# Kernel tuning notes

Measured on AMD Instinct MI355X. Metric: run time of the kernel, lower is better.

Reference implementation:

```python
import jax, jax.numpy as jnp
import numpy as np

H, N_PATCH, F, DIM = 12, 196, 8, 768
DH = DIM // H            # 64
D3 = 3 * DH              # per-head dim after 3*dim projection = 192
SCALE = float(np.sqrt(DH) * H)
B, S = 8, 1 + N_PATCH * F  # 1569


def setup_inputs() -> dict:
    key = jax.random.key(0)
    ks = jax.random.split(key, 12)
    w = lambda k, shp: (jax.random.normal(k, shp, dtype=jnp.float32) * 0.02)
    return {
        "x": jax.random.normal(ks[0], (B, S, DIM), dtype=jnp.float32),
        "Wq": w(ks[1], (DIM, 3 * DIM)), "bq": jnp.zeros((3 * DIM,), jnp.float32),
        "Wk": w(ks[2], (DIM, 3 * DIM)), "bk": jnp.zeros((3 * DIM,), jnp.float32),
        "Wv": w(ks[3], (DIM, 3 * DIM)), "bv": jnp.zeros((3 * DIM,), jnp.float32),
        "Wt": w(ks[4], (3 * DIM, DIM)), "bt": jnp.zeros((DIM,), jnp.float32),
        "Wf": w(ks[5], (3 * DIM, DIM)), "bf": jnp.zeros((DIM,), jnp.float32),
    }


def _heads(t):
    # [b, s, 3*dim] -> [b, H, s, D3]
    b, s, _ = t.shape
    return t.reshape(b, s, H, D3).transpose(0, 2, 1, 3)


def _merge(t):
    # [b, H, s, D3] -> [b, s, 3*dim]
    b, _, s, _ = t.shape
    return t.transpose(0, 2, 1, 3).reshape(b, s, H * D3)


def _attn(q, k, v):
    a = jax.nn.softmax(jnp.einsum('bhqd,bhkd->bhqk', q, k) / SCALE, axis=-1)
    return jnp.einsum('bhqk,bhkd->bhqd', a, v)


def reference(x, Wq, bq, Wk, bk, Wv, bv, Wt, bt, Wf, bf):
    patches = x[:, 1:, :]                       # [b, n*F, dim]
    # NOTE: faithful to original code: v_mat comes from self.k, k_mat from self.v
    qm = _heads(patches @ Wq + bq)
    vm = _heads(patches @ Wk + bk)
    km = _heads(patches @ Wv + bv)

    # CLS attention over full sequence (here v from self.v, k from self.k)
    q_cls = _heads(x[:, 0:1, :] @ Wq + bq)      # [b,H,1,D3]
    v_cls = _heads(x @ Wv + bv)
    k_cls = _heads(x @ Wk + bk)
    inter_cls = _attn(q_cls, k_cls, v_cls)      # [b,H,1,D3]

    # Stage 1: temporal attention per patch (patches 1..n-1), vectorized.
    # tokens are frame-major: index = frame*n + patch, so slice p::n == patch p across frames
    def per_patch(t):
        b = t.shape[0]
        return t.reshape(b, H, F, N_PATCH, D3)[:, :, :, 1:, :].transpose(0, 1, 3, 2, 4)  # [b,H,n-1,F,D3]
    q5, k5, v5 = per_patch(qm), per_patch(km), per_patch(vm)
    a1 = jax.nn.softmax(jnp.einsum('bhpfd,bhpgd->bhpfg', q5, k5) / SCALE, axis=-1)
    t1 = jnp.einsum('bhpfg,bhpgd->bhpfd', a1, v5).sum(axis=3)   # [b,H,n-1,D3]
    t1 = jnp.tile(t1, (1, 1, F, 1))                              # [b,H,(n-1)*F,D3]
    ti = _merge(t1) @ Wt + bt                                    # [b,(n-1)*F,dim]

    # Stage 2 (same qkv swap as stage 1)
    q2 = _heads(ti @ Wq + bq)
    v2 = _heads(ti @ Wk + bk)
    k2 = _heads(ti @ Wv + bv)
    outs = [_attn(q2[:, :, 0:N_PATCH], k2[:, :, 0:N_PATCH], v2[:, :, 0:N_PATCH]).sum(axis=2, keepdims=True)]
    for xi in range(1, F):  # small fixed loop over num_frames
        o = _attn(q2[:, :, xi:xi + N_PATCH], k2[:, :, xi::N_PATCH], v2[:, :, xi::N_PATCH])
        outs.append(o.sum(axis=2, keepdims=True))
    t2 = jnp.concatenate(outs, axis=2)                           # [b,H,F,D3]
    t2 = jnp.tile(t2, (1, 1, N_PATCH, 1))                        # [b,H,F*n,D3]

    full = jnp.concatenate([inter_cls, t2], axis=2)              # [b,H,1+n*F,D3]
    return _merge(full) @ Wf + bf                                # [b,S,dim]
```

## Files before the change

### kernel.cpp

```cpp
#include <hip/hip_runtime.h>
#include <math.h>

#define B_    8
#define SEQ   1569
#define DIMX  768
#define H_    12
#define D3    192
#define F_    8
#define NP    196
#define P1    195
#define NCOL  2304
#define NS    6912
#define RSCALE (1.0f/96.0f)
#define NCHUNK 16
#define CH     99
#define CLS_STRIDE 196
#define PG4   49

typedef __bf16 bf16_t;
typedef bf16_t bf16x8 __attribute__((ext_vector_type(8)));
typedef float  f32x4  __attribute__((ext_vector_type(4)));

__device__ __forceinline__ void load_lds16(const bf16_t* g, bf16_t* l) {
  __builtin_amdgcn_global_load_lds(
      (const __attribute__((address_space(1))) void*)g,
      (__attribute__((address_space(3))) void*)l, 16, 0, 0);
}

__device__ __forceinline__ float block_max256(float v, float* red) {
  #pragma unroll
  for (int o = 32; o > 0; o >>= 1) v = fmaxf(v, __shfl_xor(v, o, 64));
  __syncthreads();
  if ((threadIdx.x & 63) == 0) red[threadIdx.x >> 6] = v;
  __syncthreads();
  return fmaxf(fmaxf(red[0], red[1]), fmaxf(red[2], red[3]));
}

__device__ __forceinline__ float block_sum256(float v, float* red) {
  #pragma unroll
  for (int o = 32; o > 0; o >>= 1) v += __shfl_xor(v, o, 64);
  __syncthreads();
  if ((threadIdx.x & 63) == 0) red[threadIdx.x >> 6] = v;
  __syncthreads();
  return red[0] + red[1] + red[2] + red[3];
}

__global__ __launch_bounds__(256) void concat_bias_kernel(
    const float* __restrict__ bq, const float* __restrict__ bk,
    const float* __restrict__ bv, float* __restrict__ qkvb) {
  const int i = blockIdx.x * 256 + threadIdx.x;
  if (i >= NS) return;
  float v;
  if (i < NCOL) v = bq[i];
  else if (i < 2 * NCOL) v = bk[i - NCOL];
  else v = bv[i - 2 * NCOL];
  qkvb[i] = v;
}

__global__ __launch_bounds__(256) void cast_swizzle(
    const float* __restrict__ x, bf16_t* __restrict__ out, int Mreal) {
  const int ms = blockIdx.x;
  const int wave = threadIdx.x >> 6, lane = threadIdx.x & 63;
  const int KP = DIMX / 32;
  int row = ms * 16 + (lane & 15);
  if (row >= Mreal) row = Mreal - 1;
  const int cb = (lane >> 4) * 8;
  const float* src = x + (size_t)row * DIMX + cb;
  bf16_t* dst = out + ((size_t)ms * KP) * 512 + lane * 8;
  for (int kp = wave; kp < KP; kp += 4) {
    const float4 a = *(const float4*)(src + kp * 32);
    const float4 b = *(const float4*)(src + kp * 32 + 4);
    bf16_t o8[8] = {(bf16_t)a.x, (bf16_t)a.y, (bf16_t)a.z, (bf16_t)a.w,
                    (bf16_t)b.x, (bf16_t)b.y, (bf16_t)b.z, (bf16_t)b.w};
    *(uint4*)(dst + (size_t)kp * 512) = *(uint4*)o8;
  }
}

__global__ __launch_bounds__(256) void transpose_all(
    const float* __restrict__ Wq, const float* __restrict__ Wk,
    const float* __restrict__ Wv, const float* __restrict__ Wt,
    const float* __restrict__ Wf, bf16_t* __restrict__ WqkvT,
    bf16_t* __restrict__ WtT, bf16_t* __restrict__ WfT) {
  __shared__ float t[32][33];
  const int bid = blockIdx.x;
  const int mat = bid / 1728, tt = bid % 1728;
  const float* W; bf16_t* WT; int Kd, Nd, nt, kt;
  if (mat < 3) {
    Kd = DIMX; Nd = NCOL;
    W = (mat == 0) ? Wq : ((mat == 1) ? Wk : Wv);
    WT = WqkvT + (size_t)mat * NCOL * DIMX;
    nt = tt % 72; kt = tt / 72;
  } else {
    Kd = NCOL; Nd = DIMX;
    W = (mat == 3) ? Wt : Wf;
    WT = (mat == 3) ? WtT : WfT;
    nt = tt % 24; kt = tt / 24;
  }
  const int bn = nt * 32, bk = kt * 32;
  const int KP = Kd >> 5;
  const int tx = threadIdx.x & 31, ty = threadIdx.x >> 5;
  #pragma unroll
  for (int i = 0; i < 32; i += 8)
    t[ty + i][tx] = W[(size_t)(bk + ty + i) * Nd + bn + tx];
  __syncthreads();
  const int k = bk + tx;
  #pragma unroll
  for (int i = 0; i < 32; i += 8) {
    const int n = bn + ty + i;
    const size_t off = ((size_t)(n >> 4) * KP + (k >> 5)) * 512 +
                       ((n & 15) + 16 * ((k >> 3) & 3)) * 8 + (k & 7);
    WT[off] = (bf16_t)t[tx][ty + i];
  }
}

__global__ __launch_bounds__(256) void gemm_mfma_bt(
    const bf16_t* __restrict__ A, const bf16_t* __restrict__ BT,
    const float* __restrict__ bias, void* __restrict__ C,
    int M, int N, int K, int MT, int NT, int GROUPM, int aSwz, int outBf16) {
  __shared__ bf16_t As[128 * 64];
  __shared__ bf16_t Bs[128 * 64];
  const int tid  = threadIdx.x;
  const int wave = tid >> 6, lane = tid & 63;

  const int pid   = blockIdx.x;
  const int npg   = GROUPM * NT;
  const int group = pid / npg;
  const int first_m = group * GROUPM;
  int gsm = MT - first_m; if (gsm > GROUPM) gsm = GROUPM;
  const int lpid  = pid % npg;
  const int m_tile = first_m + lpid % gsm;
  const int n_tile = lpid / gsm;
  const int row0 = m_tile * 128, col0 = n_tile * 128;

  const int KP = K >> 5;
  const bf16_t* Bpan = BT + ((size_t)(n_tile * 8 + wave * 2) * KP) * 512 + lane * 8;
  const bf16_t* Apan = A + ((size_t)(m_tile * 8 + wave * 2) * KP) * 512 + lane * 8;
  const int fr = lane & 15, kg = lane >> 4;
  int ra0 = row0 + wave * 32 + fr;
  int ra1 = ra0 + 16;
  if (ra0 >= M) ra0 = M - 1;
  if (ra1 >= M) ra1 = M - 1;
  const bf16_t* Ap0 = A + (size_t)ra0 * K + kg * 8;
  const bf16_t* Ap1 = A + (size_t)ra1 * K + kg * 8;

  const int la0 = (wave * 2 + 0) * 1024, la1 = (wave * 2 + 1) * 1024;
  const int mb = (wave & 1) * 4,  nb = (wave >> 1) * 4;
  const int m0 = (wave & 1) * 64, n0 = (wave >> 1) * 64;
  f32x4 acc[4][4] = {};

  for (int kk = 0; kk < K; kk += 64) {
    const int kp = kk >> 5;
    if (aSwz) {
      load_lds16(Apan + (size_t)kp * 512,            &As[la0]);
      load_lds16(Apan + (size_t)(kp + 1) * 512,      &As[la0 + 512]);
      load_lds16(Apan + (size_t)(KP + kp) * 512,     &As[la1]);
      load_lds16(Apan + (size_t)(KP + kp + 1) * 512, &As[la1 + 512]);
    } else {
      load_lds16(Ap0 + kk,      &As[la0]);
      load_lds16(Ap0 + kk + 32, &As[la0 + 512]);
      load_lds16(Ap1 + kk,      &As[la1]);
      load_lds16(Ap1 + kk + 32, &As[la1 + 512]);
    }
    load_lds16(Bpan + (size_t)kp * 512,            &Bs[la0]);
    load_lds16(Bpan + (size_t)(kp + 1) * 512,      &Bs[la0 + 512]);
    load_lds16(Bpan + (size_t)(KP + kp) * 512,     &Bs[la1]);
    load_lds16(Bpan + (size_t)(KP + kp + 1) * 512, &Bs[la1 + 512]);
    __syncthreads();

    #pragma unroll
    for (int h = 0; h < 2; ++h) {
      bf16x8 af[4], bfr[4];
      #pragma unroll
      for (int i = 0; i < 4; ++i) {
        af[i]  = *(const bf16x8*)&As[(mb + i) * 1024 + h * 512 + lane * 8];
        bfr[i] = *(const bf16x8*)&Bs[(nb + i) * 1024 + h * 512 + lane * 8];
      }
      #pragma unroll
      for (int i = 0; i < 4; ++i)
        #pragma unroll
        for (int j = 0; j < 4; ++j)
          acc[i][j] = __builtin_amdgcn_mfma_f32_16x16x32_bf16(
              af[i], bfr[j], acc[i][j], 0, 0, 0);
    }
    __syncthreads();
  }

  const int cc = lane & 15, cr4 = (lane >> 4) * 4;
  #pragma unroll
  for (int i = 0; i < 4; ++i) {
    #pragma unroll
    for (int j = 0; j < 4; ++j) {
      const int col = col0 + n0 + j * 16 + cc;
      const float bcol = bias[col];
      #pragma unroll
      for (int reg = 0; reg < 4; ++reg) {
        const int r = row0 + m0 + i * 16 + cr4 + reg;
        if (r < M) {
          const float v = acc[i][j][reg] + bcol;
          if (outBf16) ((bf16_t*)C)[(size_t)r * N + col] = (bf16_t)v;
          else         ((float*)C)[(size_t)r * N + col] = v;
        }
      }
    }
  }
}

__global__ __launch_bounds__(256) void xi0_scores_mfma(
    const bf16_t* __restrict__ QKV2, float* __restrict__ Smat) {
  __shared__ bf16_t As[128 * 32];
  __shared__ bf16_t Bs[128 * 32];
  const int tid  = threadIdx.x;
  const int wave = tid >> 6, lane = tid & 63;
  const int row0 = blockIdx.x * 128, col0 = blockIdx.y * 128;
  const int bh = blockIdx.z;
  const int b = bh / H_, h = bh % H_;
  const bf16_t* Abase = QKV2 + (size_t)b * P1 * NS + h * D3;
  const bf16_t* Bbase = QKV2 + (size_t)b * P1 * NS + 2 * NCOL + h * D3;

  const int fr = lane & 15, kg = lane >> 4;
  int ra0 = row0 + wave * 32 + fr;
  int ra1 = ra0 + 16;
  if (ra0 >= P1) ra0 = P1 - 1;
  if (ra1 >= P1) ra1 = P1 - 1;
  int cb0 = col0 + wave * 32 + fr;
  int cb1 = cb0 + 16;
  if (cb0 >= P1) cb0 = P1 - 1;
  if (cb1 >= P1) cb1 = P1 - 1;
  const bf16_t* Ap0 = Abase + (size_t)ra0 * NS + kg * 8;
  const bf16_t* Ap1 = Abase + (size_t)ra1 * NS + kg * 8;
  const bf16_t* Bp0 = Bbase + (size_t)cb0 * NS + kg * 8;
  const bf16_t* Bp1 = Bbase + (size_t)cb1 * NS + kg * 8;
  bf16_t* lA0 = &As[(wave * 2 + 0) * 512];
  bf16_t* lA1 = &As[(wave * 2 + 1) * 512];
  bf16_t* lB0 = &Bs[(wave * 2 + 0) * 512];
  bf16_t* lB1 = &Bs[(wave * 2 + 1) * 512];

  const int m0 = (wave & 1) * 64, n0 = (wave >> 1) * 64;
  const int mb = (wave & 1) * 4,  nb = (wave >> 1) * 4;
  f32x4 acc[4][4] = {};

  for (int k0 = 0; k0 < D3; k0 += 32) {
    load_lds16(Ap0 + k0, lA0);
    load_lds16(Ap1 + k0, lA1);
    load_lds16(Bp0 + k0, lB0);
    load_lds16(Bp1 + k0, lB1);
    __syncthreads();
    bf16x8 af[4], bfr[4];
    #pragma unroll
    for (int i = 0; i < 4; ++i) {
      af[i]  = *(const bf16x8*)&As[(mb + i) * 512 + lane * 8];
      bfr[i] = *(const bf16x8*)&Bs[(nb + i) * 512 + lane * 8];
    }
    #pragma unroll
    for (int i = 0; i < 4; ++i)
      #pragma unroll
      for (int j = 0; j < 4; ++j)
        acc[i][j] = __builtin_amdgcn_mfma_f32_16x16x32_bf16(
            af[i], bfr[j], acc[i][j], 0, 0, 0);
    __syncthreads();
  }

  float* S = Smat + (size_t)bh * P1 * P1;
  const int cc = lane & 15, cr4 = (lane >> 4) * 4;
  #pragma unroll
  for (int i = 0; i < 4; ++i)
    #pragma unroll
    for (int j = 0; j < 4; ++j) {
      const int col = col0 + n0 + j * 16 + cc;
      #pragma unroll
      for (int reg = 0; reg < 4; ++reg) {
        const int r = row0 + m0 + i * 16 + cr4 + reg;
        if (r < P1 && col < P1) S[(size_t)r * P1 + col] = acc[i][j][reg] * RSCALE;
      }
    }
}

__global__ __launch_bounds__(256) void xi0_finish_kernel(
    const float* __restrict__ Smat, const bf16_t* __restrict__ QKV2,
    bf16_t* __restrict__ FULL9b) {
  const int bh = blockIdx.x;
  const int b = bh / H_, h = bh % H_;
  __shared__ float mrow[P1], inv_l[P1], g[P1];
  const float* S = Smat + (size_t)bh * P1 * P1;
  const int tid = threadIdx.x;
  const int wave = tid >> 6, lane = tid & 63;

  for (int r = wave; r < P1; r += 4) {
    const float* Sr = S + (size_t)r * P1;
    const float s0 = Sr[lane];
    const float s1 = Sr[64 + lane];
    const float s2 = Sr[128 + lane];
    const float s3 = (lane < 3) ? Sr[192 + lane] : -1e30f;
    float m = fmaxf(fmaxf(s0, s1), fmaxf(s2, s3));
    #pragma unroll
    for (int o = 1; o < 64; o <<= 1) m = fmaxf(m, __shfl_xor(m, o, 64));
    float e = expf(s0 - m) * ((lane == 0) ? 2.f : 1.f) + expf(s1 - m) +
              expf(s2 - m) + ((lane < 3) ? expf(s3 - m) : 0.f);
    #pragma unroll
    for (int o = 1; o < 64; o <<= 1) e += __shfl_xor(e, o, 64);
    if (lane == 0) {
      mrow[r] = m;
      inv_l[r] = ((r == 0) ? 2.f : 1.f) / e;
    }
  }
  __syncthreads();
  if (tid < P1) {
    float s = 0.f;
    for (int r = 0; r < P1; ++r)
      s += expf(S[(size_t)r * P1 + tid] - mrow[r]) * inv_l[r];
    g[tid] = s * ((tid == 0) ? 2.f : 1.f);
  }
  __syncthreads();
  if (tid < D3) {
    float acc = 0.f;
    const bf16_t* vbase = QKV2 + (size_t)b * P1 * NS + NCOL + h * D3 + tid;
    for (int k = 0; k < P1; ++k)
      acc = fmaf(g[k], (float)vbase[(size_t)k * NS], acc);
    FULL9b[((size_t)b * 9 + 1) * NCOL + h * D3 + tid] = (bf16_t)acc;
  }
}

__global__ __launch_bounds__(256) void cls_part_kernel(
    const bf16_t* __restrict__ XQKV, float* __restrict__ CLSP, int b0) {
  const int h  = blockIdx.x % H_;
  const int bl = blockIdx.x / H_;
  const int b  = b0 + bl;
  const int c  = blockIdx.y;
  const int t0 = c * CH;
  const int tend = (t0 + CH < SEQ) ? t0 + CH : SEQ;
  __shared__ float qs[D3];
  __shared__ float sc[CH];
  __shared__ float red[4];
  const int tid = threadIdx.x;

  const bf16_t* Qr = XQKV + (size_t)bl * SEQ * NS + h * D3;
  if (tid < 24) {
    const bf16x8 q8 = *(const bf16x8*)(Qr + tid * 8);
    #pragma unroll
    for (int m2 = 0; m2 < 8; ++m2) qs[tid * 8 + m2] = (float)q8[m2];
  }
  __syncthreads();

  float lmax = -1e30f;
  for (int t = t0 + tid; t < tend; t += 256) {
    const bf16_t* kr = XQKV + ((size_t)bl * SEQ + t) * NS + NCOL + h * D3;
    float acc = 0.f;
    #pragma unroll 3
    for (int d = 0; d < D3; d += 8) {
      const bf16x8 k8 = *(const bf16x8*)(kr + d);
      #pragma unroll
      for (int m2 = 0; m2 < 8; ++m2) acc = fmaf(qs[d + m2], (float)k8[m2], acc);
    }
    acc *= RSCALE;
    sc[t - t0] = acc;
    lmax = fmaxf(lmax, acc);
  }
  const float m = block_max256(lmax, red);
  float lsum = 0.f;
  for (int t = t0 + tid; t < tend; t += 256) {
    const float e = expf(sc[t - t0] - m);
    sc[t - t0] = e;
    lsum += e;
  }
  const float L = block_sum256(lsum, red);
  __syncthreads();

  float* P = CLSP + ((size_t)(b * H_ + h) * NCHUNK + c) * CLS_STRIDE;
  if (tid < D3) {
    float acc = 0.f;
    const bf16_t* vbase = XQKV + ((size_t)bl * SEQ + t0) * NS + 2 * NCOL + h * D3 + tid;
    for (int t = t0; t < tend; ++t)
      acc = fmaf(sc[t - t0], (float)vbase[(size_t)(t - t0) * NS], acc);
    P[tid] = acc;
  }
  if (tid == 192) P[192] = m;
  if (tid == 193) P[193] = L;
}

__global__ __launch_bounds__(256) void cls_combine_kernel(
    const float* __restrict__ CLSP, bf16_t* __restrict__ FULL9b) {
  const int bh = blockIdx.x;
  const int tid = threadIdx.x;
  const float* P = CLSP + (size_t)bh * NCHUNK * CLS_STRIDE;

  float M = -1e30f;
  #pragma unroll
  for (int c = 0; c < NCHUNK; ++c) M = fmaxf(M, P[c * CLS_STRIDE + 192]);
  float L = 0.f;
  float w[NCHUNK];
  #pragma unroll
  for (int c = 0; c < NCHUNK; ++c) {
    w[c] = expf(P[c * CLS_STRIDE + 192] - M);
    L += P[c * CLS_STRIDE + 193] * w[c];
  }
  if (tid < D3) {
    float acc = 0.f;
    #pragma unroll
    for (int c = 0; c < NCHUNK; ++c)
      acc = fmaf(w[c], P[c * CLS_STRIDE + tid], acc);
    const int b = bh / H_, h = bh % H_;
    FULL9b[((size_t)b * 9 + 0) * NCOL + h * D3 + tid] = (bf16_t)(acc / L);
  }
}

__global__ __launch_bounds__(256) void temporal_kernel(
    const bf16_t* __restrict__ XQKV, bf16_t* __restrict__ T1U, int b0) {
  const int id = blockIdx.x;
  const int pg = id % PG4;
  const int h  = (id / PG4) % H_;
  const int bl = id / (PG4 * H_);
  const int b  = b0 + bl;
  const int wave = threadIdx.x >> 6, lane = threadIdx.x & 63;
  __shared__ float qs[4][8][196], ks[4][8][196];

  int pi = pg * 4 + wave;
  const bool act = (pi < P1);
  if (!act) pi = P1 - 1;

  #pragma unroll
  for (int i = 0; i < 6; ++i) {
    const int idx = lane + 64 * i;
    const int arr = idx / 192;
    const int c = idx % 192;
    const int f = c / 24, d0 = (c % 24) * 8;
    const size_t base = ((size_t)bl * SEQ + (size_t)f * NP + pi + 2) * NS +
                        (arr ? 2 * NCOL : 0) + h * D3 + d0;
    const bf16x8 v8 = *(const bf16x8*)(XQKV + base);
    float* dst = arr ? &ks[wave][f][d0] : &qs[wave][f][d0];
    #pragma unroll
    for (int m2 = 0; m2 < 8; ++m2) dst[m2] = (float)v8[m2];
  }
  __syncthreads();

  const int f = lane >> 3, g = lane & 7;
  float s = 0.f;
  for (int d = 0; d < D3; d += 4) {
    const float4 a4 = *(const float4*)&qs[wave][f][d];
    const float4 b4 = *(const float4*)&ks[wave][g][d];
    s = fmaf(a4.x, b4.x, s); s = fmaf(a4.y, b4.y, s);
    s = fmaf(a4.z, b4.z, s); s = fmaf(a4.w, b4.w, s);
  }
  s *= RSCALE;

  float m = s;
  #pragma unroll
  for (int o = 1; o < 8; o <<= 1) m = fmaxf(m, __shfl_xor(m, o, 64));
  const float e = expf(s - m);
  float sum = e;
  #pragma unroll
  for (int o = 1; o < 8; o <<= 1) sum += __shfl_xor(sum, o, 64);
  float a = e / sum;
  #pragma unroll
  for (int o = 8; o < 64; o <<= 1) a += __shfl_xor(a, o, 64);
  float wg[8];
  #pragma unroll
  for (int gg = 0; gg < 8; ++gg) wg[gg] = __shfl(a, gg, 64);

  if (act) {
    const size_t vrow = (size_t)bl * SEQ * NS + NCOL + h * D3;
    #pragma unroll
    for (int i = 0; i < 3; ++i) {
      const int d = lane + 64 * i;
      float o = 0.f;
      #pragma unroll
      for (int gg = 0; gg < 8; ++gg) {
        const bf16_t vv = XQKV[vrow + ((size_t)gg * NP + pi + 2) * NS + d];
        o = fmaf(wg[gg], (float)vv, o);
      }
      T1U[((size_t)b * P1 + pi) * NCOL + h * D3 + d] = (bf16_t)o;
    }
  }
}

__global__ __launch_bounds__(256) void stage2_xi_kernel(
    const bf16_t* __restrict__ QKV2, bf16_t* __restrict__ FULL9b) {
  const int xi = 1 + blockIdx.x % 7;
  const int h  = (blockIdx.x / 7) % H_;
  const int b  = blockIdx.x / (7 * H_);
  __shared__ float Ks[8][196], Vs[8][196], Qs[32][196];
  __shared__ float Pp[32][8];
  const int tid = threadIdx.x;

  for (int idx = tid; idx < 192; idx += 256) {
    const int k = idx / 24, d0 = (idx % 24) * 8;
    const bf16x8 v8 = *(const bf16x8*)(QKV2 + ((size_t)(b * P1 + xi + k)) * NS +
                                       2 * NCOL + h * D3 + d0);
    #pragma unroll
    for (int m2 = 0; m2 < 8; ++m2) Ks[k][d0 + m2] = (float)v8[m2];
  }
  for (int idx = tid; idx < 192; idx += 256) {
    const int k = idx / 24, d0 = (idx % 24) * 8;
    const bf16x8 v8 = *(const bf16x8*)(QKV2 + ((size_t)(b * P1 + xi + k)) * NS +
                                       NCOL + h * D3 + d0);
    #pragma unroll
    for (int m2 = 0; m2 < 8; ++m2) Vs[k][d0 + m2] = (float)v8[m2];
  }

  float acc = 0.f;
  for (int c = 0; c < 7; ++c) {
    __syncthreads();
    for (int idx = tid; idx < 768; idx += 256) {
      const int qr = idx / 24, d0 = (idx % 24) * 8;
      const int rq = c * 32 + qr;
      if (rq < P1) {
        const bf16x8 v8 = *(const bf16x8*)(QKV2 + ((size_t)(b * P1 + rq)) * NS +
                                           h * D3 + d0);
        #pragma unroll
        for (int m2 = 0; m2 < 8; ++m2) Qs[qr][d0 + m2] = (float)v8[m2];
      } else {
        #pragma unroll
        for (int m2 = 0; m2 < 8; ++m2) Qs[qr][d0 + m2] = 0.f;
      }
    }
    __syncthreads();
    const int grp = tid >> 3, k = tid & 7;
    float dot = 0.f;
    for (int d = 0; d < D3; d += 4) {
      const float4 a4 = *(const float4*)&Qs[grp][d];
      const float4 b4 = *(const float4*)&Ks[k][d];
      dot = fmaf(a4.x, b4.x, dot); dot = fmaf(a4.y, b4.y, dot);
      dot = fmaf(a4.z, b4.z, dot); dot = fmaf(a4.w, b4.w, dot);
    }
    dot *= RSCALE;
    float m = dot;
    #pragma unroll
    for (int o = 1; o < 8; o <<= 1) m = fmaxf(m, __shfl_xor(m, o, 64));
    const float e = expf(dot - m);
    float s = e;
    #pragma unroll
    for (int o = 1; o < 8; o <<= 1) s += __shfl_xor(s, o, 64);
    Pp[grp][k] = e / s;
    __syncthreads();
    if (tid < D3) {
      #pragma unroll 4
      for (int g2 = 0; g2 < 32; ++g2) {
        const int rq2 = c * 32 + g2;
        if (rq2 < P1) {
          const float mult = (rq2 == xi) ? 2.f : 1.f;
          float o = 0.f;
          #pragma unroll
          for (int kk = 0; kk < 8; ++kk) o = fmaf(Pp[g2][kk], Vs[kk][tid], o);
          acc = fmaf(mult, o, acc);
        }
      }
    }
  }
  if (tid < D3)
    FULL9b[((size_t)b * 9 + 1 + xi) * NCOL + h * D3 + tid] = (bf16_t)acc;
}

__global__ __launch_bounds__(256) void bcast_kernel(
    const float* __restrict__ OUT9, float* __restrict__ out) {
  const int idx = blockIdx.x * 256 + threadIdx.x;
  const int total = B_ * SEQ * (DIMX / 4);
  if (idx >= total) return;
  const int d4 = idx % (DIMX / 4);
  const int bs = idx / (DIMX / 4);
  const int s = bs % SEQ;
  const int b = bs / SEQ;
  const int row = (s == 0) ? 0 : 1 + ((s - 1) & 7);
  ((float4*)out)[idx] = ((const float4*)OUT9)[(size_t)(b * 9 + row) * (DIMX / 4) + d4];
}

extern "C" void kernel_launch(void* const* d_in, const int* in_sizes, int n_in,
                              void* d_out, int out_size, void* d_ws, size_t ws_size,
                              hipStream_t stream) {
  const float* x  = (const float*)d_in[0];
  const float* Wq = (const float*)d_in[1];
  const float* bq = (const float*)d_in[2];
  const float* Wk = (const float*)d_in[3];
  const float* bk = (const float*)d_in[4];
  const float* Wv = (const float*)d_in[5];
  const float* bv = (const float*)d_in[6];
  const float* Wt = (const float*)d_in[7];
  const float* bt = (const float*)d_in[8];
  const float* Wf = (const float*)d_in[9];
  const float* bf = (const float*)d_in[10];
  float* out = (float*)d_out;
  (void)in_sizes; (void)n_in; (void)out_size;

  char* ws = (char*)d_ws;
  size_t off = 0;
  auto alloc_f32 = [&](size_t elems) {
    size_t a = (off + 63) & ~(size_t)63;
    off = a + elems * sizeof(float);
    return (float*)(ws + a);
  };
  auto alloc_bf16 = [&](size_t elems) {
    size_t a = (off + 63) & ~(size_t)63;
    off = a + elems * sizeof(bf16_t);
    return (bf16_t*)(ws + a);
  };

  bf16_t* T1Ub   = alloc_bf16((size_t)B_ * P1 * NCOL);
  bf16_t* TIUb   = alloc_bf16((size_t)B_ * P1 * DIMX);
  bf16_t* QKV2b  = alloc_bf16((size_t)B_ * P1 * NS);
  bf16_t* FULL9b = alloc_bf16((size_t)B_ * 9 * NCOL);
  float*  OUT9   = alloc_f32((size_t)B_ * 9 * DIMX);
  float*  Smat   = alloc_f32((size_t)B_ * H_ * P1 * P1);
  float*  CLSP   = alloc_f32((size_t)B_ * H_ * NCHUNK * CLS_STRIDE);
  float*  QKVbias= alloc_f32(NS);
  bf16_t* WqkvT  = alloc_bf16((size_t)3 * NCOL * DIMX);
  bf16_t* WtT    = alloc_bf16((size_t)DIMX * NCOL);
  bf16_t* WfT    = alloc_bf16((size_t)DIMX * NCOL);

  const size_t remain = (ws_size > off) ? (ws_size - off) : 0;
  int Bc = 8;
  while (Bc > 1 &&
         (size_t)(Bc * SEQ + 128) * (NS + DIMX) * sizeof(bf16_t) + 512 > remain)
    Bc >>= 1;
  const int MTmax = (Bc * SEQ + 127) / 128;
  bf16_t* XQKVb = alloc_bf16((size_t)Bc * SEQ * NS);
  bf16_t* xb    = alloc_bf16((size_t)MTmax * 128 * DIMX);

  transpose_all<<<dim3(1728 * 5), 256, 0, stream>>>(
      Wq, Wk, Wv, Wt, Wf, WqkvT, WtT, WfT);
  concat_bias_kernel<<<dim3((NS + 255) / 256), 256, 0, stream>>>(bq, bk, bv, QKVbias);

  for (int b0 = 0; b0 < B_; b0 += Bc) {
    const int Mrows = Bc * SEQ;
    const int MT = (Mrows + 127) / 128, NT = NS / 128;
    cast_swizzle<<<dim3(MT * 8), 256, 0, stream>>>(
        x + (size_t)b0 * SEQ * DIMX, xb, Mrows);
    gemm_mfma_bt<<<dim3(MT * NT), 256, 0, stream>>>(
        xb, WqkvT, QKVbias, XQKVb, Mrows, NS, DIMX, MT, NT, 8, 1, 1);
    cls_part_kernel<<<dim3(Bc * H_, NCHUNK), 256, 0, stream>>>(XQKVb, CLSP, b0);
    temporal_kernel<<<dim3(Bc * H_ * PG4), 256, 0, stream>>>(XQKVb, T1Ub, b0);
  }
  cls_combine_kernel<<<dim3(B_ * H_), 256, 0, stream>>>(CLSP, FULL9b);

  {
    const int MT = (B_ * P1 + 127) / 128, NT = DIMX / 128;
    gemm_mfma_bt<<<dim3(MT * NT), 256, 0, stream>>>(
        T1Ub, WtT, bt, TIUb, B_ * P1, DIMX, NCOL, MT, NT, 4, 0, 1);
  }
  {
    const int MT = (B_ * P1 + 127) / 128, NT = NS / 128;
    gemm_mfma_bt<<<dim3(MT * NT), 256, 0, stream>>>(
        TIUb, WqkvT, QKVbias, QKV2b, B_ * P1, NS, DIMX, MT, NT, 4, 0, 1);
  }

  xi0_scores_mfma<<<dim3(2, 2, B_ * H_), 256, 0, stream>>>(QKV2b, Smat);
  xi0_finish_kernel<<<dim3(B_ * H_), 256, 0, stream>>>(Smat, QKV2b, FULL9b);
  stage2_xi_kernel<<<dim3(B_ * H_ * 7), 256, 0, stream>>>(QKV2b, FULL9b);

  {
    const int MT = 1, NT = DIMX / 128;
    gemm_mfma_bt<<<dim3(MT * NT), 256, 0, stream>>>(
        FULL9b, WfT, bf, OUT9, B_ * 9, DIMX, NCOL, MT, NT, 1, 0, 0);
  }

  {
    const int total4 = B_ * SEQ * (DIMX / 4);
    bcast_kernel<<<dim3((total4 + 255) / 256), 256, 0, stream>>>(OUT9, out);
  }
}
```

Measured before the change: 669.2 us.

## Add XCD-aware tile mapping to GEMMs and emit Wt GEMM output pre-swizzled

```diff
diff --git a/kernel.cpp b/kernel.cpp
--- a/kernel.cpp
+++ b/kernel.cpp
@@ -116,20 +116,35 @@
 __global__ __launch_bounds__(256) void gemm_mfma_bt(
     const bf16_t* __restrict__ A, const bf16_t* __restrict__ BT,
     const float* __restrict__ bias, void* __restrict__ C,
-    int M, int N, int K, int MT, int NT, int GROUPM, int aSwz, int outBf16) {
+    int M, int N, int K, int MT, int NT, int GROUPM, int XCDB,
+    int aSwz, int outMode) {
   __shared__ bf16_t As[128 * 64];
   __shared__ bf16_t Bs[128 * 64];
   const int tid  = threadIdx.x;
   const int wave = tid >> 6, lane = tid & 63;
 
-  const int pid   = blockIdx.x;
-  const int npg   = GROUPM * NT;
-  const int group = pid / npg;
-  const int first_m = group * GROUPM;
-  int gsm = MT - first_m; if (gsm > GROUPM) gsm = GROUPM;
-  const int lpid  = pid % npg;
-  const int m_tile = first_m + lpid % gsm;
-  const int n_tile = lpid / gsm;
+  int m_tile, n_tile;
+  const int pid = blockIdx.x;
+  if (XCDB > 0) {
+    const int xcd = pid & 7, q = pid >> 3;
+    m_tile = xcd * XCDB + q % XCDB;
+    n_tile = q / XCDB;
+    if (m_tile >= MT) return;
+  } else if (XCDB < 0) {
+    const int nb2 = -XCDB;
+    const int xcd = pid & 7, q = pid >> 3;
+    n_tile = xcd * nb2 + q % nb2;
+    m_tile = q / nb2;
+    if (n_tile >= NT) return;
+  } else {
+    const int npg   = GROUPM * NT;
+    const int group = pid / npg;
+    const int first_m = group * GROUPM;
+    int gsm = MT - first_m; if (gsm > GROUPM) gsm = GROUPM;
+    const int lpid  = pid % npg;
+    m_tile = first_m + lpid % gsm;
+    n_tile = lpid / gsm;
+  }
   const int row0 = m_tile * 128, col0 = n_tile * 128;
 
   const int KP = K >> 5;
@@ -186,6 +201,7 @@
   }
 
   const int cc = lane & 15, cr4 = (lane >> 4) * 4;
+  const int KP2 = N >> 5;
   #pragma unroll
   for (int i = 0; i < 4; ++i) {
     #pragma unroll
@@ -197,8 +213,15 @@
         const int r = row0 + m0 + i * 16 + cr4 + reg;
         if (r < M) {
           const float v = acc[i][j][reg] + bcol;
-          if (outBf16) ((bf16_t*)C)[(size_t)r * N + col] = (bf16_t)v;
-          else         ((float*)C)[(size_t)r * N + col] = v;
+          if (outMode == 0) {
+            ((float*)C)[(size_t)r * N + col] = v;
+          } else if (outMode == 1) {
+            ((bf16_t*)C)[(size_t)r * N + col] = (bf16_t)v;
+          } else {
+            const size_t off = ((size_t)(r >> 4) * KP2 + (col >> 5)) * 512 +
+                               ((r & 15) + 16 * ((col >> 3) & 3)) * 8 + (col & 7);
+            ((bf16_t*)C)[off] = (bf16_t)v;
+          }
         }
       }
     }
@@ -593,7 +616,7 @@
   };
 
   bf16_t* T1Ub   = alloc_bf16((size_t)B_ * P1 * NCOL);
-  bf16_t* TIUb   = alloc_bf16((size_t)B_ * P1 * DIMX);
+  bf16_t* TIUb   = alloc_bf16((size_t)1664 * DIMX);
   bf16_t* QKV2b  = alloc_bf16((size_t)B_ * P1 * NS);
   bf16_t* FULL9b = alloc_bf16((size_t)B_ * 9 * NCOL);
   float*  OUT9   = alloc_f32((size_t)B_ * 9 * DIMX);
@@ -620,10 +643,11 @@
   for (int b0 = 0; b0 < B_; b0 += Bc) {
     const int Mrows = Bc * SEQ;
     const int MT = (Mrows + 127) / 128, NT = NS / 128;
+    const int XCDB = (MT + 7) / 8;
     cast_swizzle<<<dim3(MT * 8), 256, 0, stream>>>(
         x + (size_t)b0 * SEQ * DIMX, xb, Mrows);
-    gemm_mfma_bt<<<dim3(MT * NT), 256, 0, stream>>>(
-        xb, WqkvT, QKVbias, XQKVb, Mrows, NS, DIMX, MT, NT, 8, 1, 1);
+    gemm_mfma_bt<<<dim3(8 * XCDB * NT), 256, 0, stream>>>(
+        xb, WqkvT, QKVbias, XQKVb, Mrows, NS, DIMX, MT, NT, 0, XCDB, 1, 1);
     cls_part_kernel<<<dim3(Bc * H_, NCHUNK), 256, 0, stream>>>(XQKVb, CLSP, b0);
     temporal_kernel<<<dim3(Bc * H_ * PG4), 256, 0, stream>>>(XQKVb, T1Ub, b0);
   }
@@ -632,12 +656,13 @@
   {
     const int MT = (B_ * P1 + 127) / 128, NT = DIMX / 128;
     gemm_mfma_bt<<<dim3(MT * NT), 256, 0, stream>>>(
-        T1Ub, WtT, bt, TIUb, B_ * P1, DIMX, NCOL, MT, NT, 4, 0, 1);
+        T1Ub, WtT, bt, TIUb, B_ * P1, DIMX, NCOL, MT, NT, 4, 0, 0, 2);
   }
   {
     const int MT = (B_ * P1 + 127) / 128, NT = NS / 128;
-    gemm_mfma_bt<<<dim3(MT * NT), 256, 0, stream>>>(
-        TIUb, WqkvT, QKVbias, QKV2b, B_ * P1, NS, DIMX, MT, NT, 4, 0, 1);
+    const int NB = (NT + 7) / 8;
+    gemm_mfma_bt<<<dim3(8 * NB * MT), 256, 0, stream>>>(
+        TIUb, WqkvT, QKVbias, QKV2b, B_ * P1, NS, DIMX, MT, NT, 0, -NB, 1, 1);
   }
 
   xi0_scores_mfma<<<dim3(2, 2, B_ * H_), 256, 0, stream>>>(QKV2b, Smat);
@@ -647,7 +672,7 @@
   {
     const int MT = 1, NT = DIMX / 128;
     gemm_mfma_bt<<<dim3(MT * NT), 256, 0, stream>>>(
-        FULL9b, WfT, bf, OUT9, B_ * 9, DIMX, NCOL, MT, NT, 1, 0, 0);
+        FULL9b, WfT, bf, OUT9, B_ * 9, DIMX, NCOL, MT, NT, 1, 0, 0, 0);
   }
 
   {
```

Result: slower. 693.5 us (+3.6%).
